# Kernel optimization log

Measured on AMD Instinct MI355X. Metric: run time of the kernel, lower is better.

The kernel has to match this reference:

```python
import jax, jax.numpy as jnp
import numpy as np


def setup_inputs() -> dict:
    key = jax.random.key(0)
    k1, k2, k3 = jax.random.split(key, 3)
    B, Cin, Cout, K, H, W = 32, 128, 128, 4, 112, 112
    x = jax.random.normal(k1, (B, Cin, H, W), dtype=jnp.float32)
    # Conv2d 1x1 weights: [K, out_ch, in_ch] (kernel dims of size 1 squeezed)
    expert_w = jax.random.normal(k2, (K, Cout, Cin), dtype=jnp.float32) * (1.0 / np.sqrt(Cin))
    gate_w = jax.random.normal(k3, (K, Cin), dtype=jnp.float32) * (1.0 / np.sqrt(Cin))
    gate_b = jnp.zeros((K,), dtype=jnp.float32)
    return {"x": x, "expert_w": expert_w, "gate_w": gate_w, "gate_b": gate_b}


def reference(x, expert_w, gate_w, gate_b):
    # Gate: global average pool -> 1x1 conv -> softmax over K
    pooled = jnp.mean(x, axis=(2, 3))                      # [B, Cin]
    logits = pooled @ gate_w.T + gate_b                    # [B, K]
    g = jax.nn.softmax(logits, axis=1)                     # [B, K]
    # Combine expert weights per sample (math-equivalent to sum_k g_k * conv_k(x))
    w_b = jnp.einsum('bk,koi->boi', g, expert_w)           # [B, Cout, Cin]
    out = jnp.einsum('boi,bihw->bohw', w_b, x)             # [B, Cout, H, W]
    return out
```

## Files before the change

kernel.cpp:

```cpp
#include <hip/hip_runtime.h>
#include <hip/hip_bf16.h>
#include <stdint.h>

#define B_    32
#define CIN   128
#define COUT  128
#define KEXP  4
#define HW_   12544
#define NT    4

typedef __attribute__((ext_vector_type(8))) short bf16x8;
typedef __attribute__((ext_vector_type(4))) float f32x4;

static __device__ __forceinline__ ushort f2bf(float f) {
    uint32_t u = __builtin_bit_cast(uint32_t, f);
    u += 0x7FFFu + ((u >> 16) & 1u);
    return (ushort)(u >> 16);
}

__global__ __launch_bounds__(256) void pool_kernel(const float* __restrict__ x,
                                                   float* __restrict__ pooled) {
    const int row = blockIdx.x;
    const float4* __restrict__ x4 = (const float4*)(x + (size_t)row * HW_);
    const int t = threadIdx.x;
    float s = 0.f;
    for (int idx = t; idx < HW_ / 4; idx += 256) {
        float4 v = x4[idx];
        s += (v.x + v.y) + (v.z + v.w);
    }
    #pragma unroll
    for (int off = 32; off > 0; off >>= 1) s += __shfl_down(s, off, 64);
    __shared__ float wsum[4];
    if ((t & 63) == 0) wsum[t >> 6] = s;
    __syncthreads();
    if (t == 0) pooled[row] = (wsum[0] + wsum[1] + wsum[2] + wsum[3]) * (1.0f / HW_);
}

__global__ __launch_bounds__(256) void gate_kernel(const float* __restrict__ pooled,
                                                   const float* __restrict__ gate_w,
                                                   const float* __restrict__ gate_b,
                                                   const float* __restrict__ expert_w,
                                                   short* __restrict__ wmix) {
    const int b = blockIdx.x;
    const int t = threadIdx.x;
    const int wid = t >> 6, lane = t & 63;
    __shared__ float logits[KEXP];
    __shared__ float gsh[KEXP];
    {
        float p0 = pooled[b * CIN + lane];
        float p1 = pooled[b * CIN + 64 + lane];
        float s = p0 * gate_w[wid * CIN + lane] + p1 * gate_w[wid * CIN + 64 + lane];
        #pragma unroll
        for (int off = 32; off > 0; off >>= 1) s += __shfl_down(s, off, 64);
        if (lane == 0) logits[wid] = s + gate_b[wid];
    }
    __syncthreads();
    if (t == 0) {
        float m = fmaxf(fmaxf(logits[0], logits[1]), fmaxf(logits[2], logits[3]));
        float e0 = expf(logits[0] - m), e1 = expf(logits[1] - m);
        float e2 = expf(logits[2] - m), e3 = expf(logits[3] - m);
        float inv = 1.f / (e0 + e1 + e2 + e3);
        gsh[0] = e0 * inv; gsh[1] = e1 * inv; gsh[2] = e2 * inv; gsh[3] = e3 * inv;
    }
    __syncthreads();
    const float g0 = gsh[0], g1 = gsh[1], g2 = gsh[2], g3 = gsh[3];
    for (int idx = t; idx < COUT * CIN; idx += 256) {
        float w = g0 * expert_w[idx]
                + g1 * expert_w[COUT * CIN + idx]
                + g2 * expert_w[2 * COUT * CIN + idx]
                + g3 * expert_w[3 * COUT * CIN + idx];
        wmix[b * COUT * CIN + idx] = (short)f2bf(w);
    }
}

__global__ __launch_bounds__(256, 4) void conv_kernel(const float* __restrict__ x,
                                                      const short* __restrict__ wmix,
                                                      float* __restrict__ out) {
    __shared__ char wlds[COUT * 256];
    __shared__ char xlds[64 * 256];
    const int b  = blockIdx.y;
    const int t  = threadIdx.x;
    const int base_p0 = blockIdx.x * (64 * NT);

    const int pg  = t & 15;
    const int cg8 = t >> 4;

    {
        const uint4* __restrict__ wsrc = (const uint4*)(wmix + (size_t)b * COUT * CIN);
        #pragma unroll
        for (int pass = 0; pass < 8; ++pass) {
            int o  = (t >> 4) + pass * 16;
            int i4 = t & 15;
            uint4 v = wsrc[o * 16 + i4];
            *(uint4*)(wlds + o * 256 + ((i4 ^ (o & 15)) << 4)) = v;
        }
    }

    float4 xv[8];
    const float* __restrict__ xbase = x + (size_t)b * CIN * HW_ + (size_t)(cg8 * 8) * HW_;
    auto load_tile = [&](int p0) {
        const float* xr = xbase + p0 + pg * 4;
        #pragma unroll
        for (int i = 0; i < 8; ++i)
            xv[i] = *(const float4*)(xr + (size_t)i * HW_);
    };
    auto write_tile = [&]() {
        #pragma unroll
        for (int j = 0; j < 4; ++j) {
            const int pix = pg * 4 + j;
            bf16x8 pk;
            #pragma unroll
            for (int i = 0; i < 8; ++i)
                pk[i] = (short)f2bf((&xv[i].x)[j]);
            *(bf16x8*)(xlds + pix * 256 + ((cg8 ^ (pix & 15)) << 4)) = pk;
        }
    };

    const int wave = t >> 6;
    const int lane = t & 63;
    const int n = lane & 15;
    const int h = lane >> 4;
    const int pixl = wave * 16 + n;

    load_tile(base_p0);
    write_tile();
    __syncthreads();

    for (int tt = 0; tt < NT; ++tt) {
        if (tt + 1 < NT) load_tile(base_p0 + (tt + 1) * 64);

        bf16x8 xfrag[4];
        #pragma unroll
        for (int kk = 0; kk < 4; ++kk)
            xfrag[kk] = *(const bf16x8*)(xlds + pixl * 256 + (((kk * 4 + h) ^ n) << 4));

        f32x4 acc[8];
        #pragma unroll
        for (int ot = 0; ot < 8; ++ot) acc[ot] = (f32x4){0.f, 0.f, 0.f, 0.f};

        #pragma unroll
        for (int ot = 0; ot < 8; ++ot) {
            const int o = ot * 16 + n;
            #pragma unroll
            for (int kk = 0; kk < 4; ++kk) {
                bf16x8 wfrag = *(const bf16x8*)(wlds + o * 256 + (((kk * 4 + h) ^ n) << 4));
                acc[ot] = __builtin_amdgcn_mfma_f32_16x16x32_bf16(xfrag[kk], wfrag, acc[ot], 0, 0, 0);
            }
        }

        __syncthreads();
        if (tt + 1 < NT) write_tile();

        float* __restrict__ ob = out + (size_t)b * COUT * HW_ + base_p0 + tt * 64
                               + wave * 16 + h * 4;
        #pragma unroll
        for (int ot = 0; ot < 8; ++ot)
            __builtin_nontemporal_store(acc[ot], (f32x4*)(ob + (size_t)(ot * 16 + n) * HW_));

        __syncthreads();
    }
}

extern "C" void kernel_launch(void* const* d_in, const int* in_sizes, int n_in,
                              void* d_out, int out_size, void* d_ws, size_t ws_size,
                              hipStream_t stream) {
    const float* x        = (const float*)d_in[0];
    const float* expert_w = (const float*)d_in[1];
    const float* gate_w   = (const float*)d_in[2];
    const float* gate_b   = (const float*)d_in[3];
    float* out = (float*)d_out;

    float* pooled = (float*)d_ws;
    short* wmix   = (short*)((char*)d_ws + 16384);

    pool_kernel<<<dim3(B_ * CIN), 256, 0, stream>>>(x, pooled);
    gate_kernel<<<dim3(B_), 256, 0, stream>>>(pooled, gate_w, gate_b, expert_w, wmix);
    conv_kernel<<<dim3(HW_ / (64 * NT), B_), 256, 0, stream>>>(x, wmix, out);
}
```

Before: 133.9 us.

## Split batch into halves for cache reuse and use per-wave private LDS tiles

```diff
diff --git a/kernel.cpp b/kernel.cpp
--- a/kernel.cpp
+++ b/kernel.cpp
@@ -8,6 +8,7 @@
 #define KEXP  4
 #define HW_   12544
 #define NT    4
+#define BHALF 16
 
 typedef __attribute__((ext_vector_type(8))) short bf16x8;
 typedef __attribute__((ext_vector_type(4))) float f32x4;
@@ -73,17 +74,14 @@
     }
 }
 
-__global__ __launch_bounds__(256, 4) void conv_kernel(const float* __restrict__ x,
+__global__ __launch_bounds__(256, 3) void conv_kernel(const float* __restrict__ x,
                                                       const short* __restrict__ wmix,
                                                       float* __restrict__ out) {
     __shared__ char wlds[COUT * 256];
-    __shared__ char xlds[64 * 256];
+    __shared__ char xlds[4][16 * 256];
     const int b  = blockIdx.y;
     const int t  = threadIdx.x;
     const int base_p0 = blockIdx.x * (64 * NT);
-
-    const int pg  = t & 15;
-    const int cg8 = t >> 4;
 
     {
         const uint4* __restrict__ wsrc = (const uint4*)(wmix + (size_t)b * COUT * CIN);
@@ -96,10 +94,19 @@
         }
     }
 
+    const int wave = t >> 6;
+    const int lane = t & 63;
+    const int pg2  = lane & 3;
+    const int cg16 = lane >> 2;
+    const int n    = lane & 15;
+    const int h    = lane >> 4;
+    char* __restrict__ xpriv = xlds[wave];
+
+    const float* __restrict__ xbase = x + (size_t)b * CIN * HW_
+                                    + (size_t)(cg16 * 8) * HW_ + wave * 16 + pg2 * 4;
     float4 xv[8];
-    const float* __restrict__ xbase = x + (size_t)b * CIN * HW_ + (size_t)(cg8 * 8) * HW_;
     auto load_tile = [&](int p0) {
-        const float* xr = xbase + p0 + pg * 4;
+        const float* xr = xbase + p0;
         #pragma unroll
         for (int i = 0; i < 8; ++i)
             xv[i] = *(const float4*)(xr + (size_t)i * HW_);
@@ -107,20 +114,14 @@
     auto write_tile = [&]() {
         #pragma unroll
         for (int j = 0; j < 4; ++j) {
-            const int pix = pg * 4 + j;
+            const int r = pg2 * 4 + j;
             bf16x8 pk;
             #pragma unroll
             for (int i = 0; i < 8; ++i)
                 pk[i] = (short)f2bf((&xv[i].x)[j]);
-            *(bf16x8*)(xlds + pix * 256 + ((cg8 ^ (pix & 15)) << 4)) = pk;
+            *(bf16x8*)(xpriv + r * 256 + ((cg16 ^ r) << 4)) = pk;
         }
     };
-
-    const int wave = t >> 6;
-    const int lane = t & 63;
-    const int n = lane & 15;
-    const int h = lane >> 4;
-    const int pixl = wave * 16 + n;
 
     load_tile(base_p0);
     write_tile();
@@ -132,7 +133,7 @@
         bf16x8 xfrag[4];
         #pragma unroll
         for (int kk = 0; kk < 4; ++kk)
-            xfrag[kk] = *(const bf16x8*)(xlds + pixl * 256 + (((kk * 4 + h) ^ n) << 4));
+            xfrag[kk] = *(const bf16x8*)(xpriv + n * 256 + (((kk * 4 + h) ^ n) << 4));
 
         f32x4 acc[8];
         #pragma unroll
@@ -148,16 +149,13 @@
             }
         }
 
-        __syncthreads();
-        if (tt + 1 < NT) write_tile();
-
         float* __restrict__ ob = out + (size_t)b * COUT * HW_ + base_p0 + tt * 64
                                + wave * 16 + h * 4;
         #pragma unroll
         for (int ot = 0; ot < 8; ++ot)
             __builtin_nontemporal_store(acc[ot], (f32x4*)(ob + (size_t)(ot * 16 + n) * HW_));
 
-        __syncthreads();
+        if (tt + 1 < NT) write_tile();
     }
 }
 
@@ -173,7 +171,16 @@
     float* pooled = (float*)d_ws;
     short* wmix   = (short*)((char*)d_ws + 16384);
 
-    pool_kernel<<<dim3(B_ * CIN), 256, 0, stream>>>(x, pooled);
-    gate_kernel<<<dim3(B_), 256, 0, stream>>>(pooled, gate_w, gate_b, expert_w, wmix);
-    conv_kernel<<<dim3(HW_ / (64 * NT), B_), 256, 0, stream>>>(x, wmix, out);
+    for (int half = 0; half < 2; ++half) {
+        const int b0 = half * BHALF;
+        pool_kernel<<<dim3(BHALF * CIN), 256, 0, stream>>>(
+            x + (size_t)b0 * CIN * HW_, pooled + b0 * CIN);
+        gate_kernel<<<dim3(BHALF), 256, 0, stream>>>(
+            pooled + b0 * CIN, gate_w, gate_b, expert_w,
+            wmix + (size_t)b0 * COUT * CIN);
+        conv_kernel<<<dim3(HW_ / (64 * NT), BHALF), 256, 0, stream>>>(
+            x + (size_t)b0 * CIN * HW_,
+            wmix + (size_t)b0 * COUT * CIN,
+            out + (size_t)b0 * COUT * HW_);
+    }
 }
```

New measurement: 185.8 us. 38.8% more time.
